# Kernel tuning notes

Measured on AMD Instinct MI355X. Metric: run time of the kernel, lower is better.

The kernel has to match this reference:

```python
import math
import jax, jax.numpy as jnp
import numpy as np

B, S, D = 8, 2048, 512
D_MODEL = 512

def setup_inputs() -> dict:
    key = jax.random.key(0)
    kq, kk, kv = jax.random.split(key, 3)
    return {
        "query": jax.random.normal(kq, (B, S, D), dtype=jnp.float32),
        "key":   jax.random.normal(kk, (B, S, D), dtype=jnp.float32),
        "value": jax.random.normal(kv, (B, S, D), dtype=jnp.float32),
    }

def reference(query, key, value):
    # scores: [B, S, S]
    scores = jnp.einsum("bqd,bkd->bqk", query, key) / math.sqrt(D_MODEL)
    k = max(1, int(scores.shape[-1] * 0.1))
    top_scores, top_idx = jax.lax.top_k(scores, k)  # [B, S, k]
    # scatter top-k scores into a zero matrix (non-topk entries stay 0,
    # and DO participate in the softmax, matching the torch code)
    b_idx = jnp.arange(scores.shape[0])[:, None, None]
    q_idx = jnp.arange(scores.shape[1])[None, :, None]
    sparse = jnp.zeros_like(scores).at[b_idx, q_idx, top_idx].set(top_scores)
    attn = jax.nn.softmax(sparse, axis=-1)
    return jnp.einsum("bqk,bkd->bqd", attn, value)
```

## Files before the change

kernel.cpp:

```cpp
#include <hip/hip_runtime.h>
#include <math.h>

#define B_ 8
#define S_ 2048
#define D_ 512
#define KTOP 204
#define QK_SCALE 0.044194173824159216f

typedef short bfrag8 __attribute__((ext_vector_type(8)));
typedef float facc4 __attribute__((ext_vector_type(4)));

__device__ __forceinline__ unsigned short f2bf(float f) {
  unsigned u = __float_as_uint(f);
  u += 0x7FFFu + ((u >> 16) & 1);
  return (unsigned short)(u >> 16);
}

__device__ __forceinline__ unsigned fkey(float f) {
  unsigned b = __float_as_uint(f);
  return (b & 0x80000000u) ? ~b : (b | 0x80000000u);
}
__device__ __forceinline__ float keyfloat(unsigned k) {
  unsigned b = (k & 0x80000000u) ? (k & 0x7FFFFFFFu) : ~k;
  return __uint_as_float(b);
}

__device__ __forceinline__ void load16(const unsigned short* g, unsigned short* l) {
  __builtin_amdgcn_global_load_lds(
      (const __attribute__((address_space(1))) void*)g,
      (__attribute__((address_space(3))) void*)l, 16, 0, 0);
}

__global__ __launch_bounds__(256) void cvt_qk(const float* __restrict__ Q,
                                              const float* __restrict__ K,
                                              unsigned short* __restrict__ Qb,
                                              unsigned short* __restrict__ Kb) {
  const float* in = blockIdx.y ? K : Q;
  unsigned short* out = blockIdx.y ? Kb : Qb;
  int i = (blockIdx.x * 256 + threadIdx.x) * 4;
  float4 v = *(const float4*)(in + i);
  ushort4 o;
  o.x = f2bf(v.x); o.y = f2bf(v.y); o.z = f2bf(v.z); o.w = f2bf(v.w);
  *(ushort4*)(out + i) = o;
}

__global__ __launch_bounds__(256) void transpose_v(const float* __restrict__ V,
                                                   unsigned short* __restrict__ VT) {
  __shared__ float tile[32][33];
  int b = blockIdx.z;
  int d0 = blockIdx.x * 32, k0 = blockIdx.y * 32;
  const float* Vb = V + (size_t)b * S_ * D_;
  unsigned short* VTb = VT + (size_t)b * D_ * S_;
  int c = threadIdx.x & 31, r = threadIdx.x >> 5;
#pragma unroll
  for (int rr = 0; rr < 32; rr += 8)
    tile[r + rr][c] = Vb[(size_t)(k0 + r + rr) * D_ + d0 + c];
  __syncthreads();
#pragma unroll
  for (int rr = 0; rr < 32; rr += 8)
    VTb[(size_t)(d0 + r + rr) * S_ + k0 + c] = f2bf(tile[c][r + rr]);
}


__device__ __forceinline__ void stage4(const unsigned short* Ab, const unsigned short* Bb,
                                       int lda, int ldb, int k0, int srow, int scol,
                                       unsigned short* dA0, unsigned short* dA1,
                                       unsigned short* dB0, unsigned short* dB1) {
  load16(Ab + (size_t)srow * lda + k0 + scol, dA0);
  load16(Ab + (size_t)(srow + 64) * lda + k0 + scol, dA1);
  load16(Bb + (size_t)srow * ldb + k0 + scol, dB0);
  load16(Bb + (size_t)(srow + 64) * ldb + k0 + scol, dB1);
}

__device__ __forceinline__ void mfma_step(const unsigned short* sA, const unsigned short* sB,
                                          int mrow, int nrow, int l15, int quad,
                                          facc4 (&acc)[4][4]) {
  bfrag8 af[4], bq[4];
#pragma unroll
  for (int i = 0; i < 4; ++i)
    af[i] = *(const bfrag8*)(sA + (mrow + 16 * i + l15) * 32 + quad * 8);
#pragma unroll
  for (int j2 = 0; j2 < 4; ++j2)
    bq[j2] = *(const bfrag8*)(sB + (nrow + 16 * j2 + l15) * 32 + quad * 8);
#pragma unroll
  for (int i = 0; i < 4; ++i)
#pragma unroll
    for (int j2 = 0; j2 < 4; ++j2)
      acc[i][j2] = __builtin_amdgcn_mfma_f32_16x16x32_bf16(af[i], bq[j2], acc[i][j2], 0, 0, 0);
}

__global__ __launch_bounds__(256) void gemm_qk(
    const unsigned short* __restrict__ A, int lda, long long astr,
    const unsigned short* __restrict__ Bm, int ldb, long long bstr,
    float* __restrict__ C, int ldc, long long cstr,
    int kdim, float scale) {
  const unsigned j = blockIdx.x + 16u * blockIdx.y + 256u * blockIdx.z;
  const unsigned bz = j & 7u;
  const unsigned q = j >> 3;
  const unsigned by = q & 15u;
  const unsigned bx = q >> 4;

  __shared__ unsigned short smA[2][128 * 32];
  __shared__ unsigned short smB[2][128 * 32];
  const int tid = threadIdx.x;
  const int wave = tid >> 6, lane = tid & 63;
  const int quad = lane >> 4, l15 = lane & 15;
  const unsigned short* Ab = A + (long long)bz * astr + (size_t)(by * 128) * lda;
  const unsigned short* Bb = Bm + (long long)bz * bstr + (size_t)(bx * 128) * ldb;
  const int srow = tid >> 2;
  const int scol = (tid & 3) * 8;
  const int so0 = wave * 512;
  const int so1 = 2048 + wave * 512;
  const int mrow = 64 * (wave >> 1);
  const int nrow = 64 * (wave & 1);

  facc4 acc[4][4];
  const facc4 fzero = {0.f, 0.f, 0.f, 0.f};
#pragma unroll
  for (int i = 0; i < 4; ++i)
#pragma unroll
    for (int j2 = 0; j2 < 4; ++j2) acc[i][j2] = fzero;

  stage4(Ab, Bb, lda, ldb, 0, srow, scol,
         smA[0] + so0, smA[0] + so1, smB[0] + so0, smB[0] + so1);
  __syncthreads();

  for (int k0 = 0; k0 < kdim; k0 += 64) {
    stage4(Ab, Bb, lda, ldb, k0 + 32, srow, scol,
           smA[1] + so0, smA[1] + so1, smB[1] + so0, smB[1] + so1);
    mfma_step(smA[0], smB[0], mrow, nrow, l15, quad, acc);
    __syncthreads();
    if (k0 + 64 < kdim)
      stage4(Ab, Bb, lda, ldb, k0 + 64, srow, scol,
             smA[0] + so0, smA[0] + so1, smB[0] + so0, smB[0] + so1);
    mfma_step(smA[1], smB[1], mrow, nrow, l15, quad, acc);
    __syncthreads();
  }

  float* Cb = C + (long long)bz * cstr;
  const int mg = by * 128 + mrow;
  const int ng = bx * 128 + nrow;
#pragma unroll
  for (int i = 0; i < 4; ++i)
#pragma unroll
    for (int j2 = 0; j2 < 4; ++j2)
#pragma unroll
      for (int r = 0; r < 4; ++r)
        Cb[(size_t)(mg + 16 * i + quad * 4 + r) * ldc + ng + 16 * j2 + l15] = acc[i][j2][r] * scale;
}

__global__ __launch_bounds__(256) void gemm_pv(
    const unsigned short* __restrict__ A, int lda, long long astr,
    const unsigned short* __restrict__ Bm, int ldb, long long bstr,
    float* __restrict__ C, int ldc, long long cstr,
    int kdim, float scale) {
  const unsigned j = blockIdx.x + 4u * blockIdx.y + 64u * blockIdx.z;
  const unsigned bz = j & 7u;
  const unsigned q = j >> 3;
  const unsigned bx = q & 3u;
  const unsigned by = q >> 2;

  __shared__ unsigned short smA[2][128 * 32];
  __shared__ unsigned short smB[2][128 * 32];
  const int tid = threadIdx.x;
  const int wave = tid >> 6, lane = tid & 63;
  const int quad = lane >> 4, l15 = lane & 15;
  const unsigned short* Ab = A + (long long)bz * astr + (size_t)(by * 128) * lda;
  const unsigned short* Bb = Bm + (long long)bz * bstr + (size_t)(bx * 128) * ldb;
  const int srow = tid >> 2;
  const int scol = (tid & 3) * 8;
  const int so0 = wave * 512;
  const int so1 = 2048 + wave * 512;
  const int mrow = 64 * (wave >> 1);
  const int nrow = 64 * (wave & 1);

  facc4 acc[4][4];
  const facc4 fzero = {0.f, 0.f, 0.f, 0.f};
#pragma unroll
  for (int i = 0; i < 4; ++i)
#pragma unroll
    for (int j2 = 0; j2 < 4; ++j2) acc[i][j2] = fzero;

  stage4(Ab, Bb, lda, ldb, 0, srow, scol,
         smA[0] + so0, smA[0] + so1, smB[0] + so0, smB[0] + so1);
  __syncthreads();

  for (int k0 = 0; k0 < kdim; k0 += 64) {
    stage4(Ab, Bb, lda, ldb, k0 + 32, srow, scol,
           smA[1] + so0, smA[1] + so1, smB[1] + so0, smB[1] + so1);
    mfma_step(smA[0], smB[0], mrow, nrow, l15, quad, acc);
    __syncthreads();
    if (k0 + 64 < kdim)
      stage4(Ab, Bb, lda, ldb, k0 + 64, srow, scol,
             smA[0] + so0, smA[0] + so1, smB[0] + so0, smB[0] + so1);
    mfma_step(smA[1], smB[1], mrow, nrow, l15, quad, acc);
    __syncthreads();
  }

  float* Cb = C + (long long)bz * cstr;
  const int mg = by * 128 + mrow;
  const int ng = bx * 128 + nrow;
#pragma unroll
  for (int i = 0; i < 4; ++i)
#pragma unroll
    for (int j2 = 0; j2 < 4; ++j2)
#pragma unroll
      for (int r = 0; r < 4; ++r)
        Cb[(size_t)(mg + 16 * i + quad * 4 + r) * ldc + ng + 16 * j2 + l15] = acc[i][j2][r] * scale;
}

__device__ __forceinline__ unsigned sel256(const unsigned* bins, int lane,
                                           unsigned krem, unsigned* krem_out) {
  const uint4 b = *(const uint4*)(bins + lane * 4);
  const unsigned s = b.x + b.y + b.z + b.w;
  unsigned t = s;
#pragma unroll
  for (int off = 1; off < 64; off <<= 1) {
    unsigned u = (unsigned)__shfl_down((int)t, off);
    t += (lane + off < 64) ? u : 0u;
  }
  const unsigned texcl = t - s;
  const unsigned c3 = texcl + b.w;
  const unsigned c2 = c3 + b.z;
  const unsigned c1 = c2 + b.y;
  const unsigned c0 = c1 + b.x;
  unsigned pack = 0;
  if (c0 >= krem && c1 < krem)    pack = ((krem - c1) << 8) | (lane * 4 + 0);
  if (c1 >= krem && c2 < krem)    pack = ((krem - c2) << 8) | (lane * 4 + 1);
  if (c2 >= krem && c3 < krem)    pack = ((krem - c3) << 8) | (lane * 4 + 2);
  if (c3 >= krem && texcl < krem) pack = ((krem - texcl) << 8) | (lane * 4 + 3);
#pragma unroll
  for (int off = 1; off < 64; off <<= 1)
    pack |= (unsigned)__shfl_xor((int)pack, off);
  *krem_out = pack >> 8;
  return pack & 255u;
}

__global__ __launch_bounds__(256) void topk_softmax(float* __restrict__ scores) {
  __shared__ unsigned binsAll[4][256];
  const int tid = threadIdx.x;
  const int wave = tid >> 6, lane = tid & 63;
  const long long row = (long long)blockIdx.x * 4 + wave;
  float* srow = scores + row * 2048;
  unsigned* bins = binsAll[wave];

  unsigned k[32];
#pragma unroll
  for (int c = 0; c < 4; ++c) {
    float4 a = *(const float4*)(srow + c * 512 + lane * 8);
    float4 b = *(const float4*)(srow + c * 512 + lane * 8 + 4);
    k[c * 8 + 0] = fkey(a.x); k[c * 8 + 1] = fkey(a.y);
    k[c * 8 + 2] = fkey(a.z); k[c * 8 + 3] = fkey(a.w);
    k[c * 8 + 4] = fkey(b.x); k[c * 8 + 5] = fkey(b.y);
    k[c * 8 + 6] = fkey(b.z); k[c * 8 + 7] = fkey(b.w);
  }

  unsigned kmax = 0;
#pragma unroll
  for (int i = 0; i < 32; ++i) kmax = max(kmax, k[i]);
#pragma unroll
  for (int off = 1; off < 64; off <<= 1)
    kmax = max(kmax, (unsigned)__shfl_xor((int)kmax, off));
  const float m = fmaxf(keyfloat(kmax), 0.f);

  {
    uint4 z; z.x = 0; z.y = 0; z.z = 0; z.w = 0;
    *(uint4*)(bins + lane * 4) = z;
  }
#pragma unroll
  for (int i = 0; i < 32; ++i) {
    const int t = (int)(k[i] >> 16) - 0xBF00;
    if (t >= 1) atomicAdd(&bins[min(t, 255)], 1u);
  }
  unsigned krem;
  const unsigned d1 = sel256(bins, lane, KTOP, &krem);

  unsigned tkey;
  if (d1 >= 1u && d1 <= 254u) {
    const unsigned top16 = 0xBF00u + d1;
    { uint4 z; z.x = 0; z.y = 0; z.z = 0; z.w = 0; *(uint4*)(bins + lane * 4) = z; }
#pragma unroll
    for (int i = 0; i < 32; ++i)
      if ((k[i] >> 16) == top16) atomicAdd(&bins[(k[i] >> 8) & 255u], 1u);
    const unsigned b1 = sel256(bins, lane, krem, &krem);
    const unsigned top24 = (top16 << 8) | b1;
    { uint4 z; z.x = 0; z.y = 0; z.z = 0; z.w = 0; *(uint4*)(bins + lane * 4) = z; }
#pragma unroll
    for (int i = 0; i < 32; ++i)
      if ((k[i] >> 8) == top24) atomicAdd(&bins[k[i] & 255u], 1u);
    const unsigned b0 = sel256(bins, lane, krem, &krem);
    tkey = (top24 << 8) | b0;
  } else {
    krem = KTOP;
    unsigned prefix = 0, mmask = 0;
    for (int shift = 24; shift >= 0; shift -= 8) {
      { uint4 z; z.x = 0; z.y = 0; z.z = 0; z.w = 0; *(uint4*)(bins + lane * 4) = z; }
#pragma unroll
      for (int i = 0; i < 32; ++i)
        if ((k[i] & mmask) == prefix) atomicAdd(&bins[(k[i] >> shift) & 255u], 1u);
      const unsigned dig = sel256(bins, lane, krem, &krem);
      prefix |= dig << shift;
      mmask |= 0xFFu << shift;
    }
    tkey = prefix;
  }

  unsigned cut;
  {
    unsigned tiem = 0;
#pragma unroll
    for (int i = 0; i < 32; ++i)
      if (k[i] == tkey) tiem |= 1u << i;
    unsigned need = krem;
    for (;;) {
      unsigned myidx = 0xFFFFFFFFu;
      if (tiem) {
        int i = __ffs((int)tiem) - 1;
        myidx = ((unsigned)(i >> 3)) * 512u + (unsigned)lane * 8u + (unsigned)(i & 7);
      }
      unsigned minidx = myidx;
#pragma unroll
      for (int off = 1; off < 64; off <<= 1)
        minidx = min(minidx, (unsigned)__shfl_xor((int)minidx, off));
      if (--need == 0 || minidx == 0xFFFFFFFFu) { cut = minidx; break; }
      if (myidx == minidx) tiem &= tiem - 1;
    }
  }

  const float eqw = __expf(keyfloat(tkey) - m);
  const float base = __expf(-m);
  float zsum = 0.f;
#pragma unroll
  for (int i = 0; i < 32; ++i) {
    const unsigned key = k[i];
    const unsigned idx = ((unsigned)(i >> 3)) * 512u + (unsigned)lane * 8u + (unsigned)(i & 7);
    float w;
    if (key > tkey) w = __expf(keyfloat(key) - m);
    else w = (key == tkey && idx <= cut) ? eqw : base;
    zsum += w;
    k[i] = __float_as_uint(w);
  }
#pragma unroll
  for (int off = 1; off < 64; off <<= 1) zsum += __shfl_xor(zsum, off);
  const float invZ = 1.f / zsum;

  unsigned short* arow = (unsigned short*)scores + row * 4096;
#pragma unroll
  for (int c = 0; c < 4; ++c) {
    union { unsigned short u[8]; int4 v4; } pk;
#pragma unroll
    for (int j = 0; j < 8; ++j)
      pk.u[j] = f2bf(__uint_as_float(k[c * 8 + j]) * invZ);
    *(int4*)(arow + c * 512 + lane * 8) = pk.v4;
  }
}

extern "C" void kernel_launch(void* const* d_in, const int* in_sizes, int n_in,
                              void* d_out, int out_size, void* d_ws, size_t ws_size,
                              hipStream_t stream) {
  const float* Q = (const float*)d_in[0];
  const float* K = (const float*)d_in[1];
  const float* V = (const float*)d_in[2];
  float* out = (float*)d_out;
  char* ws = (char*)d_ws;
  unsigned short* Qb = (unsigned short*)(ws);
  unsigned short* Kb = (unsigned short*)(ws + ((size_t)16 << 20));
  unsigned short* VT = (unsigned short*)(ws + ((size_t)32 << 20));
  float* scores = (float*)(ws + ((size_t)48 << 20));

  const int nel = B_ * S_ * D_;
  cvt_qk<<<dim3(nel / 1024, 2), 256, 0, stream>>>(Q, K, Qb, Kb);
  transpose_v<<<dim3(D_ / 32, S_ / 32, B_), 256, 0, stream>>>(V, VT);
  gemm_qk<<<dim3(S_ / 128, S_ / 128, B_), 256, 0, stream>>>(
      Qb, D_, (long long)S_ * D_, Kb, D_, (long long)S_ * D_,
      scores, S_, (long long)S_ * S_, D_, QK_SCALE);
  topk_softmax<<<B_ * S_ / 4, 256, 0, stream>>>(scores);
  gemm_pv<<<dim3(D_ / 128, S_ / 128, B_), 256, 0, stream>>>(
      (const unsigned short*)scores, 4096, (long long)S_ * 4096,
      VT, S_, (long long)D_ * S_, out, D_, (long long)S_ * D_, S_, 1.0f);
}
```

Measured before the change: 286.0 us.

## Triple-buffer LDS staging in QK and PV GEMMs with vmcnt-based waits

Both bf16 GEMM kernels move from a double-buffered LDS pipeline to a three-stage ring buffer. Two tiles are kept in flight, and the full __syncthreads is replaced by an s_waitcnt vmcnt(4) plus barrier, so the wave waits only on the older tile's loads. This aims to hide more global-to-LDS load latency behind the MFMA work. In exchange it uses more LDS per block, which may lower occupancy, and it relies on the async load16 behaviour being counted by vmcnt.

```diff
diff --git a/kernel.cpp b/kernel.cpp
--- a/kernel.cpp
+++ b/kernel.cpp
@@ -62,14 +62,13 @@
 }
 
 
-__device__ __forceinline__ void stage4(const unsigned short* Ab, const unsigned short* Bb,
-                                       int lda, int ldb, int k0, int srow, int scol,
-                                       unsigned short* dA0, unsigned short* dA1,
-                                       unsigned short* dB0, unsigned short* dB1) {
-  load16(Ab + (size_t)srow * lda + k0 + scol, dA0);
-  load16(Ab + (size_t)(srow + 64) * lda + k0 + scol, dA1);
-  load16(Bb + (size_t)srow * ldb + k0 + scol, dB0);
-  load16(Bb + (size_t)(srow + 64) * ldb + k0 + scol, dB1);
+__device__ __forceinline__ void stageAB(const unsigned short* Ab, const unsigned short* Bb,
+                                        int lda, int ldb, int k0, int srow, int scol,
+                                        int wave, unsigned short* bA, unsigned short* bB) {
+  load16(Ab + (size_t)srow * lda + k0 + scol, bA + wave * 512);
+  load16(Ab + (size_t)(srow + 64) * lda + k0 + scol, bA + 2048 + wave * 512);
+  load16(Bb + (size_t)srow * ldb + k0 + scol, bB + wave * 512);
+  load16(Bb + (size_t)(srow + 64) * ldb + k0 + scol, bB + 2048 + wave * 512);
 }
 
 __device__ __forceinline__ void mfma_step(const unsigned short* sA, const unsigned short* sB,
@@ -88,6 +87,11 @@
     for (int j2 = 0; j2 < 4; ++j2)
       acc[i][j2] = __builtin_amdgcn_mfma_f32_16x16x32_bf16(af[i], bq[j2], acc[i][j2], 0, 0, 0);
 }
+
+#define PHASE_WAIT(N)                                   \
+  asm volatile("s_waitcnt vmcnt(" #N ")" ::: "memory"); \
+  __builtin_amdgcn_s_barrier();                         \
+  __builtin_amdgcn_sched_barrier(0)
 
 __global__ __launch_bounds__(256) void gemm_qk(
     const unsigned short* __restrict__ A, int lda, long long astr,
@@ -100,8 +104,8 @@
   const unsigned by = q & 15u;
   const unsigned bx = q >> 4;
 
-  __shared__ unsigned short smA[2][128 * 32];
-  __shared__ unsigned short smB[2][128 * 32];
+  __shared__ unsigned short smA[3][128 * 32];
+  __shared__ unsigned short smB[3][128 * 32];
   const int tid = threadIdx.x;
   const int wave = tid >> 6, lane = tid & 63;
   const int quad = lane >> 4, l15 = lane & 15;
@@ -109,8 +113,6 @@
   const unsigned short* Bb = Bm + (long long)bz * bstr + (size_t)(bx * 128) * ldb;
   const int srow = tid >> 2;
   const int scol = (tid & 3) * 8;
-  const int so0 = wave * 512;
-  const int so1 = 2048 + wave * 512;
   const int mrow = 64 * (wave >> 1);
   const int nrow = 64 * (wave & 1);
 
@@ -121,21 +123,24 @@
 #pragma unroll
     for (int j2 = 0; j2 < 4; ++j2) acc[i][j2] = fzero;
 
-  stage4(Ab, Bb, lda, ldb, 0, srow, scol,
-         smA[0] + so0, smA[0] + so1, smB[0] + so0, smB[0] + so1);
-  __syncthreads();
-
-  for (int k0 = 0; k0 < kdim; k0 += 64) {
-    stage4(Ab, Bb, lda, ldb, k0 + 32, srow, scol,
-           smA[1] + so0, smA[1] + so1, smB[1] + so0, smB[1] + so1);
-    mfma_step(smA[0], smB[0], mrow, nrow, l15, quad, acc);
-    __syncthreads();
-    if (k0 + 64 < kdim)
-      stage4(Ab, Bb, lda, ldb, k0 + 64, srow, scol,
-             smA[0] + so0, smA[0] + so1, smB[0] + so0, smB[0] + so1);
-    mfma_step(smA[1], smB[1], mrow, nrow, l15, quad, acc);
-    __syncthreads();
-  }
+  unsigned short *A0 = smA[0], *A1 = smA[1], *A2 = smA[2];
+  unsigned short *B0 = smB[0], *B1 = smB[1], *B2 = smB[2];
+
+  stageAB(Ab, Bb, lda, ldb, 0, srow, scol, wave, A0, B0);
+  stageAB(Ab, Bb, lda, ldb, 32, srow, scol, wave, A1, B1);
+  PHASE_WAIT(4);
+
+  const int T = kdim >> 5;
+  for (int t = 0; t < T - 2; ++t) {
+    stageAB(Ab, Bb, lda, ldb, (t + 2) * 32, srow, scol, wave, A2, B2);
+    mfma_step(A0, B0, mrow, nrow, l15, quad, acc);
+    PHASE_WAIT(4);
+    unsigned short* tA = A0; A0 = A1; A1 = A2; A2 = tA;
+    unsigned short* tB = B0; B0 = B1; B1 = B2; B2 = tB;
+  }
+  mfma_step(A0, B0, mrow, nrow, l15, quad, acc);
+  PHASE_WAIT(0);
+  mfma_step(A1, B1, mrow, nrow, l15, quad, acc);
 
   float* Cb = C + (long long)bz * cstr;
   const int mg = by * 128 + mrow;
@@ -160,8 +165,8 @@
   const unsigned bx = q & 3u;
   const unsigned by = q >> 2;
 
-  __shared__ unsigned short smA[2][128 * 32];
-  __shared__ unsigned short smB[2][128 * 32];
+  __shared__ unsigned short smA[3][128 * 32];
+  __shared__ unsigned short smB[3][128 * 32];
   const int tid = threadIdx.x;
   const int wave = tid >> 6, lane = tid & 63;
   const int quad = lane >> 4, l15 = lane & 15;
@@ -169,8 +174,6 @@
   const unsigned short* Bb = Bm + (long long)bz * bstr + (size_t)(bx * 128) * ldb;
   const int srow = tid >> 2;
   const int scol = (tid & 3) * 8;
-  const int so0 = wave * 512;
-  const int so1 = 2048 + wave * 512;
   const int mrow = 64 * (wave >> 1);
   const int nrow = 64 * (wave & 1);
 
@@ -181,21 +184,24 @@
 #pragma unroll
     for (int j2 = 0; j2 < 4; ++j2) acc[i][j2] = fzero;
 
-  stage4(Ab, Bb, lda, ldb, 0, srow, scol,
-         smA[0] + so0, smA[0] + so1, smB[0] + so0, smB[0] + so1);
-  __syncthreads();
-
-  for (int k0 = 0; k0 < kdim; k0 += 64) {
-    stage4(Ab, Bb, lda, ldb, k0 + 32, srow, scol,
-           smA[1] + so0, smA[1] + so1, smB[1] + so0, smB[1] + so1);
-    mfma_step(smA[0], smB[0], mrow, nrow, l15, quad, acc);
-    __syncthreads();
-    if (k0 + 64 < kdim)
-      stage4(Ab, Bb, lda, ldb, k0 + 64, srow, scol,
-             smA[0] + so0, smA[0] + so1, smB[0] + so0, smB[0] + so1);
-    mfma_step(smA[1], smB[1], mrow, nrow, l15, quad, acc);
-    __syncthreads();
-  }
+  unsigned short *A0 = smA[0], *A1 = smA[1], *A2 = smA[2];
+  unsigned short *B0 = smB[0], *B1 = smB[1], *B2 = smB[2];
+
+  stageAB(Ab, Bb, lda, ldb, 0, srow, scol, wave, A0, B0);
+  stageAB(Ab, Bb, lda, ldb, 32, srow, scol, wave, A1, B1);
+  PHASE_WAIT(4);
+
+  const int T = kdim >> 5;
+  for (int t = 0; t < T - 2; ++t) {
+    stageAB(Ab, Bb, lda, ldb, (t + 2) * 32, srow, scol, wave, A2, B2);
+    mfma_step(A0, B0, mrow, nrow, l15, quad, acc);
+    PHASE_WAIT(4);
+    unsigned short* tA = A0; A0 = A1; A1 = A2; A2 = tA;
+    unsigned short* tB = B0; B0 = B1; B1 = B2; B2 = tB;
+  }
+  mfma_step(A0, B0, mrow, nrow, l15, quad, acc);
+  PHASE_WAIT(0);
+  mfma_step(A1, B1, mrow, nrow, l15, quad, acc);
 
   float* Cb = C + (long long)bz * cstr;
   const int mg = by * 128 + mrow;
```

Result: faster. 280.4 us (-2.0%).
